# Optimization experiments

Measured on AMD Instinct MI355X. Metric: run time of the kernel, lower is better.

The kernel has to match this reference:

```python
import jax, jax.numpy as jnp
import numpy as np

N_SAMPLES = 524288
N_FEATURES = 64
N_GATES = 64
N_OUTPUTS = 8
BASE = N_FEATURES + 2                # X cols + constant-0 col + constant-1 col
MAX_CONN = BASE + N_GATES            # 130
TEMPERATURE = 1.0                    # forward() default
NEG = -1e9                           # mask value for not-yet-available slots


def setup_inputs() -> dict:
    key = jax.random.key(0)
    k1, k2, k3 = jax.random.split(key, 3)
    X = jax.random.uniform(k1, (N_SAMPLES, N_FEATURES), dtype=jnp.float32)
    gate_weights = jax.random.normal(k2, (N_GATES, MAX_CONN), dtype=jnp.float32) * 0.1
    output_weights = jax.random.normal(k3, (N_GATES, N_OUTPUTS), dtype=jnp.float32) * 0.1
    output_scale = jnp.ones((N_OUTPUTS,), dtype=jnp.float32)
    return {"X": X, "gate_weights": gate_weights,
            "output_weights": output_weights, "output_scale": output_scale}


def reference(X, gate_weights, output_weights, output_scale):
    n = X.shape[0]
    # available = [X | zeros | ones | gate slots]; gate slots filled sequentially
    buf = jnp.concatenate([
        X,
        jnp.zeros((n, 1), X.dtype),
        jnp.ones((n, 1), X.dtype),
        jnp.zeros((n, N_GATES), X.dtype),
    ], axis=1)                                            # [N, MAX_CONN]

    # Connection selection is data-independent: softmax over the first
    # (BASE + gate_idx) slots of each gate's weight row, then top-2.
    col_ids = jnp.arange(MAX_CONN)
    avail_mask = col_ids[None, :] < (BASE + jnp.arange(N_GATES))[:, None]
    logits = jnp.where(avail_mask, gate_weights / TEMPERATURE, NEG)
    probs = jax.nn.softmax(logits, axis=1)                # [n_gates, MAX_CONN]
    _, top2 = jax.lax.top_k(probs, 2)                     # [n_gates, 2]

    # Sequential NAND chain over a small fixed number of gates (structural loop).
    gate_outs = []
    for i in range(N_GATES):
        a = buf[:, top2[i, 0]]                            # [N]
        b = buf[:, top2[i, 1]]
        g = 1.0 - a * b                                   # continuous NAND
        gate_outs.append(g)
        buf = buf.at[:, BASE + i].set(g)

    gate_matrix = jnp.stack(gate_outs, axis=1)            # [N, n_gates]
    outputs = (gate_matrix @ output_weights) * output_scale
    return outputs
```

## Files before the change

### kernel.cpp

```cpp
#include <hip/hip_runtime.h>
#include <hip/hip_fp16.h>

#define N_SAMPLES 524288
#define N_FEATURES 64
#define N_GATES 64
#define N_OUTPUTS 8
#define BASE_COLS 66
#define MAX_CONN 130

#define TPB 256
#define NW 128
#define STR 129

__device__ inline void top2_ins(float x, int j, float& v1, int& i1, float& v2, int& i2) {
    bool gt1 = (x > v1) || (x == v1 && j < i1);
    bool gt2 = (x > v2) || (x == v2 && j < i2);
    if (gt1) { v2 = v1; i2 = i1; v1 = x; i1 = j; }
    else if (gt2) { v2 = x; i2 = j; }
}

__global__ __launch_bounds__(64) void topk_prep_kernel(const float* __restrict__ gw,
                                                       int2* __restrict__ gidx) {
    const int i = blockIdx.x;
    const int l = threadIdx.x;
    const float* w = gw + i * MAX_CONN;
    const int avail = BASE_COLS + i;

    float v1 = -1e30f, v2 = -1e30f;
    int   i1 = 0x7fffffff, i2 = 0x7fffffff;
    for (int s = 0; s < 3; ++s) {
        int j = l + 64 * s;
        if (j < avail) top2_ins(w[j], j, v1, i1, v2, i2);
    }
    #pragma unroll
    for (int d = 1; d < 64; d <<= 1) {
        float ov1 = __shfl_xor(v1, d);
        int   oi1 = __shfl_xor(i1, d);
        float ov2 = __shfl_xor(v2, d);
        int   oi2 = __shfl_xor(i2, d);
        top2_ins(ov1, oi1, v1, i1, v2, i2);
        top2_ins(ov2, oi2, v1, i1, v2, i2);
    }
    if (l == 0) gidx[i] = make_int2(i1, i2);
}

__global__ __launch_bounds__(NW) void circuit_kernel(
    const float* __restrict__ X,
    const int2*  __restrict__ gidx,
    const float* __restrict__ ow,
    const float* __restrict__ scale,
    float*       __restrict__ out)
{
    __shared__ __half2 buf[MAX_CONN * STR];

    const int t = threadIdx.x;
    const long long s0 = (long long)blockIdx.x * TPB;

    const float4* Xv = (const float4*)(X + s0 * N_FEATURES);
    #pragma unroll
    for (int k = 0; k < 16; ++k) {
        int q  = k * NW + t;
        int c4 = q & 15;
        int j  = q >> 4;
        float4 va = Xv[(2 * j)     * 16 + c4];
        float4 vb = Xv[(2 * j + 1) * 16 + c4];
        int c = 4 * c4;
        buf[(c + 0) * STR + j] = __halves2half2(__float2half(va.x), __float2half(vb.x));
        buf[(c + 1) * STR + j] = __halves2half2(__float2half(va.y), __float2half(vb.y));
        buf[(c + 2) * STR + j] = __halves2half2(__float2half(va.z), __float2half(vb.z));
        buf[(c + 3) * STR + j] = __halves2half2(__float2half(va.w), __float2half(vb.w));
    }
    buf[64 * STR + t] = __halves2half2(__float2half(0.0f), __float2half(0.0f));
    buf[65 * STR + t] = __halves2half2(__float2half(1.0f), __float2half(1.0f));
    __syncthreads();

    float acc0[N_OUTPUTS], acc1[N_OUTPUTS];
    #pragma unroll
    for (int o = 0; o < N_OUTPUTS; ++o) { acc0[o] = 0.0f; acc1[o] = 0.0f; }

    const __half2 one2 = __halves2half2(__float2half(1.0f), __float2half(1.0f));

    #pragma unroll
    for (int i = 0; i < N_GATES; ++i) {
        int2 p = gidx[i];
        __half2 a = buf[p.x * STR + t];
        __half2 b = buf[p.y * STR + t];
        __half2 g = __hfma2(__hneg2(a), b, one2);
        buf[(BASE_COLS + i) * STR + t] = g;
        float g0 = __low2float(g);
        float g1 = __high2float(g);
        #pragma unroll
        for (int o = 0; o < N_OUTPUTS; ++o) {
            float w = ow[i * N_OUTPUTS + o];
            acc0[o] = fmaf(g0, w, acc0[o]);
            acc1[o] = fmaf(g1, w, acc1[o]);
        }
    }

    float sc[N_OUTPUTS];
    #pragma unroll
    for (int o = 0; o < N_OUTPUTS; ++o) sc[o] = scale[o];

    float4* outv = (float4*)(out + (s0 + 2 * t) * N_OUTPUTS);
    outv[0] = make_float4(acc0[0] * sc[0], acc0[1] * sc[1], acc0[2] * sc[2], acc0[3] * sc[3]);
    outv[1] = make_float4(acc0[4] * sc[4], acc0[5] * sc[5], acc0[6] * sc[6], acc0[7] * sc[7]);
    outv[2] = make_float4(acc1[0] * sc[0], acc1[1] * sc[1], acc1[2] * sc[2], acc1[3] * sc[3]);
    outv[3] = make_float4(acc1[4] * sc[4], acc1[5] * sc[5], acc1[6] * sc[6], acc1[7] * sc[7]);
}

extern "C" void kernel_launch(void* const* d_in, const int* in_sizes, int n_in,
                              void* d_out, int out_size, void* d_ws, size_t ws_size,
                              hipStream_t stream) {
    const float* X     = (const float*)d_in[0];
    const float* gw    = (const float*)d_in[1];
    const float* ow    = (const float*)d_in[2];
    const float* scale = (const float*)d_in[3];
    float* out = (float*)d_out;

    int2* gidx = (int2*)d_ws;

    topk_prep_kernel<<<N_GATES, 64, 0, stream>>>(gw, gidx);

    int blocks = N_SAMPLES / TPB;
    circuit_kernel<<<blocks, NW, 0, stream>>>(X, gidx, ow, scale, out);
}
```

Baseline: 217.3 us.

## Group independent gates into padded chunks and accumulate outputs in half2

Adds a planning kernel that splits the gate chain into runs of mutually independent gates, padded to groups of eight, so the circuit kernel can issue all LDS loads of a group before computing and storing it. This exposes more instruction-level parallelism than the strictly serial per-gate chain. The output projection moves from fp32 FMAs to packed half2 FMAs with weights pre-converted to duplicated half pairs, halving that arithmetic at a cost in accumulation precision. The gate loop now depends on a runtime chunk count and per-chunk entries read from global memory, and the planning kernel adds a small extra single-block launch.

```diff
diff --git a/kernel.cpp b/kernel.cpp
--- a/kernel.cpp
+++ b/kernel.cpp
@@ -7,10 +7,16 @@
 #define N_OUTPUTS 8
 #define BASE_COLS 66
 #define MAX_CONN 130
+#define NCOLS 131
 
 #define TPB 256
 #define NW 128
 #define STR 129
+
+#define WS_GIDX   0
+#define WS_NCHK   512
+#define WS_OWH2   1024
+#define WS_ENT    4096
 
 __device__ inline void top2_ins(float x, int j, float& v1, int& i1, float& v2, int& i2) {
     bool gt1 = (x > v1) || (x == v1 && j < i1);
@@ -44,17 +50,58 @@
     if (l == 0) gidx[i] = make_int2(i1, i2);
 }
 
+__global__ __launch_bounds__(64) void plan_kernel(const int2* __restrict__ gidx,
+                                                  const float* __restrict__ ow,
+                                                  char* __restrict__ ws) {
+    __shared__ int spa[N_GATES], spb[N_GATES];
+    const int t = threadIdx.x;
+
+    unsigned int* owh = (unsigned int*)(ws + WS_OWH2);
+    int4* ent = (int4*)(ws + WS_ENT);
+    int*  nchk = (int*)(ws + WS_NCHK);
+
+    int2 p = gidx[t];
+    spa[t] = p.x; spb[t] = p.y;
+
+    #pragma unroll
+    for (int o = 0; o < N_OUTPUTS; ++o) {
+        unsigned short u = __half_as_ushort(__float2half(ow[t * N_OUTPUTS + o]));
+        owh[t * N_OUTPUTS + o] = (unsigned int)u * 0x10001u;
+    }
+    if (t < N_OUTPUTS) owh[N_GATES * N_OUTPUTS + t] = 0u;
+
+    __syncthreads();
+
+    if (t == 0) {
+        int i = 0, e = 0;
+        while (i < N_GATES) {
+            int cs = i;
+            int limit = BASE_COLS + cs;
+            while (i < N_GATES && spa[i] < limit && spb[i] < limit) ++i;
+            for (int j = cs; j < i; ++j)
+                ent[e++] = make_int4(spa[j] * STR, spb[j] * STR,
+                                     (BASE_COLS + j) * STR, j);
+            while (e & 7)
+                ent[e++] = make_int4(64 * STR, 64 * STR, 130 * STR, N_GATES);
+        }
+        *nchk = e >> 3;
+    }
+}
+
 __global__ __launch_bounds__(NW) void circuit_kernel(
     const float* __restrict__ X,
-    const int2*  __restrict__ gidx,
-    const float* __restrict__ ow,
+    const char*  __restrict__ ws,
     const float* __restrict__ scale,
     float*       __restrict__ out)
 {
-    __shared__ __half2 buf[MAX_CONN * STR];
+    __shared__ __half2 buf[NCOLS * STR];
 
     const int t = threadIdx.x;
     const long long s0 = (long long)blockIdx.x * TPB;
+
+    const int4* ent = (const int4*)(ws + WS_ENT);
+    const unsigned int* owh = (const unsigned int*)(ws + WS_OWH2);
+    const int nc = *(const int*)(ws + WS_NCHK);
 
     const float4* Xv = (const float4*)(X + s0 * N_FEATURES);
     #pragma unroll
@@ -74,26 +121,34 @@
     buf[65 * STR + t] = __halves2half2(__float2half(1.0f), __float2half(1.0f));
     __syncthreads();
 
-    float acc0[N_OUTPUTS], acc1[N_OUTPUTS];
+    const __half2 one2 = __halves2half2(__float2half(1.0f), __float2half(1.0f));
+    __half2 acc[N_OUTPUTS];
     #pragma unroll
-    for (int o = 0; o < N_OUTPUTS; ++o) { acc0[o] = 0.0f; acc1[o] = 0.0f; }
+    for (int o = 0; o < N_OUTPUTS; ++o) acc[o] = __halves2half2(__float2half(0.0f), __float2half(0.0f));
 
-    const __half2 one2 = __halves2half2(__float2half(1.0f), __float2half(1.0f));
+    for (int c = 0; c < nc; ++c) {
+        int4 E[8];
+        #pragma unroll
+        for (int j = 0; j < 8; ++j) E[j] = ent[c * 8 + j];
 
-    #pragma unroll
-    for (int i = 0; i < N_GATES; ++i) {
-        int2 p = gidx[i];
-        __half2 a = buf[p.x * STR + t];
-        __half2 b = buf[p.y * STR + t];
-        __half2 g = __hfma2(__hneg2(a), b, one2);
-        buf[(BASE_COLS + i) * STR + t] = g;
-        float g0 = __low2float(g);
-        float g1 = __high2float(g);
+        __half2 av[8], bv[8];
         #pragma unroll
-        for (int o = 0; o < N_OUTPUTS; ++o) {
-            float w = ow[i * N_OUTPUTS + o];
-            acc0[o] = fmaf(g0, w, acc0[o]);
-            acc1[o] = fmaf(g1, w, acc1[o]);
+        for (int j = 0; j < 8; ++j) {
+            av[j] = buf[E[j].x + t];
+            bv[j] = buf[E[j].y + t];
+        }
+        __half2 gv[8];
+        #pragma unroll
+        for (int j = 0; j < 8; ++j) {
+            gv[j] = __hfma2(__hneg2(av[j]), bv[j], one2);
+            buf[E[j].z + t] = gv[j];
+        }
+        #pragma unroll
+        for (int j = 0; j < 8; ++j) {
+            const __half2* wrow = (const __half2*)(owh + E[j].w * N_OUTPUTS);
+            #pragma unroll
+            for (int o = 0; o < N_OUTPUTS; ++o)
+                acc[o] = __hfma2(gv[j], wrow[o], acc[o]);
         }
     }
 
@@ -101,11 +156,17 @@
     #pragma unroll
     for (int o = 0; o < N_OUTPUTS; ++o) sc[o] = scale[o];
 
+    float a0[N_OUTPUTS], a1[N_OUTPUTS];
+    #pragma unroll
+    for (int o = 0; o < N_OUTPUTS; ++o) {
+        a0[o] = __low2float(acc[o])  * sc[o];
+        a1[o] = __high2float(acc[o]) * sc[o];
+    }
     float4* outv = (float4*)(out + (s0 + 2 * t) * N_OUTPUTS);
-    outv[0] = make_float4(acc0[0] * sc[0], acc0[1] * sc[1], acc0[2] * sc[2], acc0[3] * sc[3]);
-    outv[1] = make_float4(acc0[4] * sc[4], acc0[5] * sc[5], acc0[6] * sc[6], acc0[7] * sc[7]);
-    outv[2] = make_float4(acc1[0] * sc[0], acc1[1] * sc[1], acc1[2] * sc[2], acc1[3] * sc[3]);
-    outv[3] = make_float4(acc1[4] * sc[4], acc1[5] * sc[5], acc1[6] * sc[6], acc1[7] * sc[7]);
+    outv[0] = make_float4(a0[0], a0[1], a0[2], a0[3]);
+    outv[1] = make_float4(a0[4], a0[5], a0[6], a0[7]);
+    outv[2] = make_float4(a1[0], a1[1], a1[2], a1[3]);
+    outv[3] = make_float4(a1[4], a1[5], a1[6], a1[7]);
 }
 
 extern "C" void kernel_launch(void* const* d_in, const int* in_sizes, int n_in,
@@ -117,10 +178,12 @@
     const float* scale = (const float*)d_in[3];
     float* out = (float*)d_out;
 
-    int2* gidx = (int2*)d_ws;
+    char* ws = (char*)d_ws;
+    int2* gidx = (int2*)(ws + WS_GIDX);
 
     topk_prep_kernel<<<N_GATES, 64, 0, stream>>>(gw, gidx);
+    plan_kernel<<<1, 64, 0, stream>>>(gidx, ow, ws);
 
     int blocks = N_SAMPLES / TPB;
-    circuit_kernel<<<blocks, NW, 0, stream>>>(X, gidx, ow, scale, out);
+    circuit_kernel<<<blocks, NW, 0, stream>>>(X, ws, scale, out);
 }
```

After: 240.9 us. +10.8%, slower.
